# Optimization experiments

Measured on AMD Instinct MI355X. Metric: run time of the kernel, lower is better.

The kernel has to match this reference:

```python
import jax, jax.numpy as jnp
import numpy as np

B, L, HID, H, DH = 1, 2048, 1024, 16, 64
KW = 2  # d_conv
EPS = float(np.finfo(np.float32).eps)  # torch RMSNorm eps=None -> dtype eps


def _causal_dw_conv(x, w, b):
    # x: (B, L, D), w: (D, K), b: (D,). Depthwise causal conv, no activation.
    Bs, Ls, D = x.shape
    K = w.shape[1]
    xp = jnp.pad(x, ((0, 0), (K - 1, 0), (0, 0)))
    out = b
    for k in range(K):
        out = out + xp[:, k:k + Ls, :] * w[:, k]
    return out


def setup_inputs() -> dict:
    key = jax.random.key(0)
    ks = jax.random.split(key, 14)
    hidden_states = jax.random.normal(ks[0], (B, L, HID), jnp.float32)
    # masked_fill(attention_mask != 0, -inf): True above diagonal (future masked)
    attention_mask = jnp.triu(jnp.ones((L, L), dtype=bool), 1)[None, None]
    all_dim = 3 * H * DH  # q_size + 2*kv_size with KVH == H
    qkv_w = jax.random.normal(ks[1], (all_dim, HID), jnp.float32) * 0.02
    q_conv_w = jax.random.normal(ks[2], (H * DH, KW), jnp.float32) * 0.5
    q_conv_b = jax.random.normal(ks[3], (H * DH,), jnp.float32) * 0.02
    k_conv_w = jax.random.normal(ks[4], (H * DH, KW), jnp.float32) * 0.5
    k_conv_b = jax.random.normal(ks[5], (H * DH,), jnp.float32) * 0.02
    v_conv_w = jax.random.normal(ks[6], (H * DH, KW), jnp.float32) * 0.5
    v_conv_b = jax.random.normal(ks[7], (H * DH,), jnp.float32) * 0.02
    norm_w = jnp.ones((DH,), jnp.float32)
    A_log = jnp.log(jax.random.uniform(ks[8], (H,), jnp.float32, 1.0, 16.0))
    dt0 = jnp.exp(jax.random.uniform(ks[9], (H,), jnp.float32)
                  * (np.log(0.1) - np.log(0.001)) + np.log(0.001))
    dt0 = jnp.clip(dt0, 1e-4)
    dt_bias = dt0 + jnp.log(-jnp.expm1(-dt0))  # inverse softplus init
    dt_proj_w = jax.random.normal(ks[10], (H, HID), jnp.float32) * 0.02
    dt_proj_b = jnp.zeros((H,), jnp.float32)
    o_w = jax.random.normal(ks[11], (HID, H * DH), jnp.float32) * 0.02
    order_coeff = jnp.ones((1, H, 1, 1), jnp.float32)  # 1/cumprod(arange(1,2))
    return dict(hidden_states=hidden_states, attention_mask=attention_mask,
                qkv_w=qkv_w, q_conv_w=q_conv_w, q_conv_b=q_conv_b,
                k_conv_w=k_conv_w, k_conv_b=k_conv_b, v_conv_w=v_conv_w,
                v_conv_b=v_conv_b, norm_w=norm_w, A_log=A_log, dt_bias=dt_bias,
                dt_proj_w=dt_proj_w, dt_proj_b=dt_proj_b, o_w=o_w,
                order_coeff=order_coeff)


def reference(hidden_states, attention_mask, qkv_w, q_conv_w, q_conv_b,
              k_conv_w, k_conv_b, v_conv_w, v_conv_b, norm_w, A_log, dt_bias,
              dt_proj_w, dt_proj_b, o_w, order_coeff):
    qs = H * DH
    qkv = hidden_states @ qkv_w.T                    # (B, L, 3*H*DH)
    q = _causal_dw_conv(qkv[..., :qs], q_conv_w, q_conv_b)
    k = _causal_dw_conv(qkv[..., qs:2 * qs], k_conv_w, k_conv_b)
    v = _causal_dw_conv(qkv[..., 2 * qs:], v_conv_w, v_conv_b)
    # split heads -> (B, H, L, DH)
    q = q.reshape(B, L, H, DH).transpose(0, 2, 1, 3)
    k = k.reshape(B, L, H, DH).transpose(0, 2, 1, 3)
    v = v.reshape(B, L, H, DH).transpose(0, 2, 1, 3)
    # SSM-style gate: dt (B, L, H)
    dt = jax.nn.softplus(hidden_states @ dt_proj_w.T + dt_proj_b + dt_bias)
    v = v * jnp.swapaxes(dt, 1, 2)[..., None]        # value scaled by dt
    A = -jnp.exp(A_log)[None, None, :] * dt          # (B, L, H)
    A_cumsum = jnp.swapaxes(jnp.cumsum(A, axis=1), 1, 2)  # (B, H, L)
    diff = A_cumsum[:, :, :, None] - A_cumsum[:, :, None, :]  # (B, H, L, L)
    A_mask = jnp.exp(jnp.where(attention_mask, -jnp.inf, diff))
    # order == 1: Taylor series reduces to a single gated linear term
    scores = jnp.einsum('bhld,bhmd->bhlm', q, k) * A_mask * (1.0 / order_coeff)
    out = scores @ v                                  # (B, H, L, DH)
    # RMSNorm over head_dim
    out = out * jax.lax.rsqrt(jnp.mean(out * out, -1, keepdims=True) + EPS) * norm_w
    out = out.transpose(0, 2, 1, 3).reshape(B, L, H * DH)
    return out @ o_w.T
```

## Files before the change

kernel.cpp:

```cpp
#include <hip/hip_runtime.h>
#include <hip/hip_bf16.h>

#define L_SEQ 2048
#define HIDN  1024
#define NH    16
#define DHD   64
#define QKV_N 3072

typedef float f4 __attribute__((ext_vector_type(4)));
typedef __bf16 bf16x8 __attribute__((ext_vector_type(8)));
typedef _Float16 half8 __attribute__((ext_vector_type(8)));
typedef unsigned int u32x2 __attribute__((ext_vector_type(2)));

union H8 {
  half8 h;
  u32x2 u2[2];
  uint4 u4;
};

__device__ __forceinline__ float b2f(unsigned short u) {
  union { unsigned int i; float f; } c; c.i = ((unsigned int)u) << 16; return c.f;
}
__device__ __forceinline__ unsigned short f2b(float f) {
  union { float f; unsigned int i; } c; c.f = f;
  unsigned int r = c.i + 0x7FFFu + ((c.i >> 16) & 1u);
  return (unsigned short)(r >> 16);
}
__device__ __forceinline__ unsigned short f2h(float f) {
  union { _Float16 h; unsigned short u; } c; c.h = (_Float16)f; return c.u;
}
__device__ __forceinline__ void unpack8(uint4 u, float* f) {
  unsigned int w[4] = {u.x, u.y, u.z, u.w};
#pragma unroll
  for (int i = 0; i < 4; ++i) {
    union { unsigned int i_; float f_; } lo, hi;
    lo.i_ = w[i] << 16;
    hi.i_ = w[i] & 0xffff0000u;
    f[2 * i] = lo.f_; f[2 * i + 1] = hi.f_;
  }
}

__global__ __launch_bounds__(256) void prep_kernel(
    const void* hs, const void* qkvw, const void* ow, const void* dtw,
    const void* qw, const void* qb, const void* kw, const void* kb,
    const void* vw, const void* vb, const void* nw, const void* al,
    const void* dtb, const void* dpb, const void* oc,
    unsigned short* __restrict__ hs_b, unsigned short* __restrict__ qkvw_b,
    unsigned short* __restrict__ ow_b, unsigned short* __restrict__ dtw_b,
    float* __restrict__ smallf, int* __restrict__ flag)
{
  __shared__ int cnt;
  if (threadIdx.x == 0) cnt = 0;
  __syncthreads();
  {
    const unsigned short* p = (const unsigned short*)hs;
    int c = 0;
    for (int i = threadIdx.x; i < 8192; i += 256)
      if (((p[i] >> 7) & 0xFFu) >= 140u) c++;
    atomicAdd(&cnt, c);
  }
  __syncthreads();
  const int f = (cnt >= 32) ? 1 : 0;
  if (blockIdx.x == 0 && threadIdx.x == 0) *flag = f;

  const int tid = blockIdx.x * 256 + threadIdx.x;
  const int nth = gridDim.x * 256;
  for (int i = tid; i < 1576960; i += nth) {
    const void* src; unsigned short* dst; int off;
    if (i < 524288)       { src = hs;   dst = hs_b;   off = i; }
    else if (i < 1310720) { src = qkvw; dst = qkvw_b; off = i - 524288; }
    else if (i < 1572864) { src = ow;   dst = ow_b;   off = i - 1310720; }
    else                  { src = dtw;  dst = dtw_b;  off = i - 1572864; }
    const int e = off * 4;
    if (f) {
      f4 v = *(const f4*)((const float*)src + e);
      ushort4 o;
      o.x = f2b(v[0]); o.y = f2b(v[1]); o.z = f2b(v[2]); o.w = f2b(v[3]);
      *(ushort4*)(dst + e) = o;
    } else {
      *(uint2*)(dst + e) = *(const uint2*)((const unsigned short*)src + e);
    }
  }
  const void* ptrs[11] = {qw, qb, kw, kb, vw, vb, nw, al, dtb, dpb, oc};
  const int sizes[11] = {2048, 1024, 2048, 1024, 2048, 1024, 64, 16, 16, 16, 16};
  int off = 0;
  for (int a = 0; a < 11; ++a) {
    for (int i = tid; i < sizes[a]; i += nth)
      smallf[off + i] = f ? ((const float*)ptrs[a])[i]
                          : b2f(((const unsigned short*)ptrs[a])[i]);
    off += sizes[a];
  }
}

__global__ __launch_bounds__(256) void gemm128(
    const unsigned short* __restrict__ A, const unsigned short* __restrict__ B,
    float* __restrict__ C, int M, int N, int K)
{
  __shared__ __align__(16) unsigned short As[128 * 40];
  __shared__ __align__(16) unsigned short Bs[128 * 40];
  const int t = threadIdx.x;
  const int w = t >> 6, lane = t & 63;
  const int quad = lane >> 4, l16 = lane & 15;
  const int wr = w >> 1, wc = w & 1;
  const int m0 = blockIdx.y * 128, n0 = blockIdx.x * 128;
  const int srow = t >> 1;
  const int scol = (t & 1) * 16;

  f4 acc[4][4];
#pragma unroll
  for (int i = 0; i < 4; ++i)
#pragma unroll
    for (int j = 0; j < 4; ++j) acc[i][j] = (f4){0.f, 0.f, 0.f, 0.f};

  const unsigned short* apg = A + (size_t)(m0 + srow) * K + scol;
  const unsigned short* bpg = B + (size_t)(n0 + srow) * K + scol;
  uint4 a0 = *(const uint4*)apg,       a1 = *(const uint4*)(apg + 8);
  uint4 b0 = *(const uint4*)bpg,       b1 = *(const uint4*)(bpg + 8);

  for (int k0 = 0; k0 < K; k0 += 32) {
    __syncthreads();
    *(uint4*)&As[srow * 40 + scol]     = a0;
    *(uint4*)&As[srow * 40 + scol + 8] = a1;
    *(uint4*)&Bs[srow * 40 + scol]     = b0;
    *(uint4*)&Bs[srow * 40 + scol + 8] = b1;
    __syncthreads();
    if (k0 + 32 < K) {
      a0 = *(const uint4*)(apg + k0 + 32); a1 = *(const uint4*)(apg + k0 + 40);
      b0 = *(const uint4*)(bpg + k0 + 32); b1 = *(const uint4*)(bpg + k0 + 40);
    }
    bf16x8 aF[4], bF[4];
#pragma unroll
    for (int i = 0; i < 4; ++i)
      aF[i] = *(const bf16x8*)&As[(wr * 64 + i * 16 + l16) * 40 + quad * 8];
#pragma unroll
    for (int j = 0; j < 4; ++j)
      bF[j] = *(const bf16x8*)&Bs[(wc * 64 + j * 16 + l16) * 40 + quad * 8];
#pragma unroll
    for (int i = 0; i < 4; ++i)
#pragma unroll
      for (int j = 0; j < 4; ++j)
        acc[i][j] = __builtin_amdgcn_mfma_f32_16x16x32_bf16(aF[i], bF[j], acc[i][j], 0, 0, 0);
  }

#pragma unroll
  for (int i = 0; i < 4; ++i)
#pragma unroll
    for (int j = 0; j < 4; ++j)
#pragma unroll
      for (int r = 0; r < 4; ++r) {
        int m = m0 + wr * 64 + i * 16 + quad * 4 + r;
        int n = n0 + wc * 64 + j * 16 + l16;
        C[(size_t)m * N + n] = acc[i][j][r];
      }
}

template <int MODE>
__global__ __launch_bounds__(256) void gemm_bt(
    const unsigned short* __restrict__ A, const unsigned short* __restrict__ B,
    void* __restrict__ Cv, int M, int N, int K, const int* __restrict__ flag)
{
  __shared__ __align__(16) short As[64 * 40];
  __shared__ __align__(16) short Bs[64 * 40];
  const int t = threadIdx.x;
  const int wave = t >> 6, lane = t & 63;
  const int quad = lane >> 4, l16 = lane & 15;
  const int m0 = blockIdx.y * 64, n0 = blockIdx.x * 64;
  const int srow = t >> 2, scol = (t & 3) * 8;
  f4 acc[4];
#pragma unroll
  for (int i = 0; i < 4; ++i) acc[i] = (f4){0.f, 0.f, 0.f, 0.f};
  const unsigned short* ap = A + (size_t)(m0 + srow) * K + scol;
  const unsigned short* bp = B + (size_t)(n0 + srow) * K + scol;
  for (int k0 = 0; k0 < K; k0 += 32) {
    uint4 av = *(const uint4*)(ap + k0);
    uint4 bv = *(const uint4*)(bp + k0);
    __syncthreads();
    *(uint4*)&As[srow * 40 + scol] = av;
    *(uint4*)&Bs[srow * 40 + scol] = bv;
    __syncthreads();
    bf16x8 af = *(const bf16x8*)&As[(wave * 16 + l16) * 40 + quad * 8];
#pragma unroll
    for (int nt = 0; nt < 4; ++nt) {
      bf16x8 bf = *(const bf16x8*)&Bs[(nt * 16 + l16) * 40 + quad * 8];
      acc[nt] = __builtin_amdgcn_mfma_f32_16x16x32_bf16(af, bf, acc[nt], 0, 0, 0);
    }
  }
  const int outf32 = (MODE == 0) ? 1 : (*flag ? 1 : 0);
#pragma unroll
  for (int nt = 0; nt < 4; ++nt) {
#pragma unroll
    for (int r = 0; r < 4; ++r) {
      int m = m0 + wave * 16 + quad * 4 + r;
      int n = n0 + nt * 16 + l16;
      if (outf32) ((float*)Cv)[(size_t)m * N + n] = acc[nt][r];
      else        ((unsigned short*)Cv)[(size_t)m * N + n] = f2b(acc[nt][r]);
    }
  }
}

__global__ __launch_bounds__(256) void dt_kernel(
    const unsigned short* __restrict__ hs,
    const unsigned short* __restrict__ dtw,
    const float* __restrict__ smallf,
    float* __restrict__ dt_out, float* __restrict__ A_out)
{
  const int l = blockIdx.x;
  const int t = threadIdx.x, wave = t >> 6, lane = t & 63;
  const unsigned short* hp = hs + (size_t)l * HIDN + lane * 16;
  float hv[16];
  unpack8(*(const uint4*)hp, hv);
  unpack8(*(const uint4*)(hp + 8), hv + 8);
#pragma unroll
  for (int hh = 0; hh < 4; ++hh) {
    const int hd = wave * 4 + hh;
    const unsigned short* wp = dtw + (size_t)hd * HIDN + lane * 16;
    float wv[16];
    unpack8(*(const uint4*)wp, wv);
    unpack8(*(const uint4*)(wp + 8), wv + 8);
    float p = 0.f;
#pragma unroll
    for (int i = 0; i < 16; ++i) p += hv[i] * wv[i];
#pragma unroll
    for (int off = 32; off > 0; off >>= 1) p += __shfl_down(p, off);
    if (lane == 0) {
      float z = p + smallf[9312 + hd] + smallf[9296 + hd];
      float dtv = (z > 20.f) ? z : log1pf(expf(z));
      dt_out[l * NH + hd] = dtv;
      A_out[l * NH + hd] = -expf(smallf[9280 + hd]) * dtv;
    }
  }
}

__global__ __launch_bounds__(64) void cumsum_kernel(const float* __restrict__ A_in,
                                                    float* __restrict__ Ac)
{
  const int h = blockIdx.x;
  const int lane = threadIdx.x;
  const int base = lane * 32;
  float run = 0.f;
  for (int i = 0; i < 32; ++i) run += A_in[(base + i) * NH + h];
  float incl = run;
#pragma unroll
  for (int off = 1; off < 64; off <<= 1) {
    float n = __shfl_up(incl, off);
    if (lane >= off) incl += n;
  }
  float r2 = incl - run;
  for (int i = 0; i < 32; ++i) {
    r2 += A_in[(base + i) * NH + h];
    Ac[h * L_SEQ + base + i] = r2;
  }
}

__global__ __launch_bounds__(256) void conv_kernel(
    const float* __restrict__ qkv, const float* __restrict__ smallf,
    const float* __restrict__ dt, unsigned short* __restrict__ qc)
{
  const int idx = blockIdx.x * 256 + threadIdx.x;
  const int l = idx / (QKV_N / 4);
  const int c = (idx % (QKV_N / 4)) * 4;
  f4 xc = *(const f4*)&qkv[(size_t)l * QKV_N + c];
  f4 xp = (f4){0.f, 0.f, 0.f, 0.f};
  if (l > 0) xp = *(const f4*)&qkv[(size_t)(l - 1) * QKV_N + c];
  const float* w; const float* b; int cb;
  if (c < HIDN)          { w = smallf;        b = smallf + 2048; cb = c; }
  else if (c < 2 * HIDN) { w = smallf + 3072; b = smallf + 5120; cb = c - HIDN; }
  else                   { w = smallf + 6144; b = smallf + 8192; cb = c - 2 * HIDN; }
  f4 o;
#pragma unroll
  for (int j = 0; j < 4; ++j)
    o[j] = b[cb + j] + xp[j] * w[(cb + j) * 2] + xc[j] * w[(cb + j) * 2 + 1];
  if (c >= 2 * HIDN) {
    const int hh = (c - 2 * HIDN) >> 6;
    o *= dt[l * NH + hh];
  }
  ushort4 st;
  st.x = f2h(o[0]); st.y = f2h(o[1]); st.z = f2h(o[2]); st.w = f2h(o[3]);
  *(ushort4*)&qc[(size_t)l * QKV_N + c] = st;
}

__global__ __launch_bounds__(256) void transpose_v(
    const unsigned short* __restrict__ qc, unsigned short* __restrict__ vt)
{
  const int h = blockIdx.y;
  const int l0 = blockIdx.x * 64;
  const int t = threadIdx.x;
  const int srow = t >> 2, cc = t & 3;
  __shared__ __align__(16) unsigned short Ts[64 * 68];
  const unsigned short* gp =
      qc + (size_t)(l0 + srow) * QKV_N + 2 * HIDN + h * DHD + cc * 16;
  uint4 a = *(const uint4*)gp;
  uint4 b = *(const uint4*)(gp + 8);
  *(uint4*)&Ts[srow * 68 + cc * 16] = a;
  *(uint4*)&Ts[srow * 68 + cc * 16 + 8] = b;
  __syncthreads();
  __align__(16) unsigned short o[16];
#pragma unroll
  for (int j = 0; j < 16; ++j) o[j] = Ts[(cc * 16 + j) * 68 + srow];
  unsigned short* op = vt + ((size_t)h * DHD + srow) * L_SEQ + l0 + cc * 16;
  *(uint4*)op = *(const uint4*)&o[0];
  *(uint4*)(op + 8) = *(const uint4*)&o[8];
}

__global__ __launch_bounds__(256) void attn_kernel(
    const unsigned short* __restrict__ qc,
    const unsigned short* __restrict__ vt,
    const float* __restrict__ Ac,
    const float* __restrict__ smallf,
    unsigned short* __restrict__ attn_out)
{
  const int h  = blockIdx.y;
  const int bx = blockIdx.x;
  const int jj = bx >> 1;
  const int base = (bx & 1) ? jj : (31 - jj);
  const int lt = (h < 8) ? base : (31 - base);
  const int t  = threadIdx.x;
  const int w    = t >> 6;
  const int lane = t & 63;
  const int l16  = lane & 15;
  const int quad = lane >> 4;
  const int srow = t >> 2;
  const int cc   = t & 3;

  __shared__ __align__(16) unsigned short K_lds[2][64 * 68];
  __shared__ __align__(16) unsigned short V_lds[2][64 * 68];
  __shared__ __align__(16) unsigned short S_lds[64 * 68];

  const int l0 = lt * 64;
  const float rc = 1.0f / smallf[9328 + h];
  const float* Acp = Ac + h * L_SEQ;

  H8 qf0, qf1;
  {
    const unsigned short* qp =
        qc + (size_t)(l0 + w * 16 + l16) * QKV_N + h * DHD + quad * 8;
    qf0.u4 = *(const uint4*)qp;
    qf1.u4 = *(const uint4*)(qp + 32);
  }
  float alv[4];
#pragma unroll
  for (int r = 0; r < 4; ++r) alv[r] = Acp[l0 + w * 16 + quad * 4 + r];

  f4 acc[4];
#pragma unroll
  for (int i = 0; i < 4; ++i) acc[i] = (f4){0.f, 0.f, 0.f, 0.f};

  const unsigned short* kgp =
      qc + (size_t)srow * QKV_N + HIDN + h * DHD + cc * 16;
  const unsigned short* vgp =
      vt + ((size_t)h * DHD + srow) * L_SEQ + cc * 16;

  const int swo = srow * 68 + cc * 16;

  uint4 k0v = *(const uint4*)kgp,       k1v = *(const uint4*)(kgp + 8);
  uint4 v0v = *(const uint4*)vgp,       v1v = *(const uint4*)(vgp + 8);
  float amv[4];
#pragma unroll
  for (int nt = 0; nt < 4; ++nt) amv[nt] = Acp[nt * 16 + l16];

  *(u32x2*)&K_lds[0][swo]      = (u32x2){k0v.x, k0v.y};
  *(u32x2*)&K_lds[0][swo + 4]  = (u32x2){k0v.z, k0v.w};
  *(u32x2*)&K_lds[0][swo + 8]  = (u32x2){k1v.x, k1v.y};
  *(u32x2*)&K_lds[0][swo + 12] = (u32x2){k1v.z, k1v.w};
  *(u32x2*)&V_lds[0][swo]      = (u32x2){v0v.x, v0v.y};
  *(u32x2*)&V_lds[0][swo + 4]  = (u32x2){v0v.z, v0v.w};
  *(u32x2*)&V_lds[0][swo + 8]  = (u32x2){v1v.x, v1v.y};
  *(u32x2*)&V_lds[0][swo + 12] = (u32x2){v1v.z, v1v.w};
  __syncthreads();

  int cur = 0;
  for (int it = 0; it <= lt; ++it) {
    uint4 nk0 = k0v, nk1 = k1v, nv0 = v0v, nv1 = v1v;
    float namv[4];
    const bool more = (it < lt);
    if (more) {
      const unsigned short* kp = kgp + (size_t)(it + 1) * 64 * QKV_N;
      const unsigned short* vp = vgp + (size_t)(it + 1) * 64;
      nk0 = *(const uint4*)kp; nk1 = *(const uint4*)(kp + 8);
      nv0 = *(const uint4*)vp; nv1 = *(const uint4*)(vp + 8);
#pragma unroll
      for (int nt = 0; nt < 4; ++nt)
        namv[nt] = Acp[(it + 1) * 64 + nt * 16 + l16];
    }

    f4 s[4];
#pragma unroll
    for (int i = 0; i < 4; ++i) s[i] = (f4){0.f, 0.f, 0.f, 0.f};
#pragma unroll
    for (int ks = 0; ks < 2; ++ks) {
      H8 qk = ks ? qf1 : qf0;
#pragma unroll
      for (int nt = 0; nt < 4; ++nt) {
        H8 kf;
        const int ko = (nt * 16 + l16) * 68 + ks * 32 + quad * 8;
        kf.u2[0] = *(const u32x2*)&K_lds[cur][ko];
        kf.u2[1] = *(const u32x2*)&K_lds[cur][ko + 4];
        s[nt] = __builtin_amdgcn_mfma_f32_16x16x32_f16(qk.h, kf.h, s[nt], 0, 0, 0);
      }
    }
    const int m0 = it * 64;
#pragma unroll
    for (int nt = 0; nt < 4; ++nt) {
      const int mg = m0 + nt * 16 + l16;
      const float am = amv[nt];
#pragma unroll
      for (int r = 0; r < 4; ++r) {
        const int lg = l0 + w * 16 + quad * 4 + r;
        float val = (mg <= lg) ? s[nt][r] * __expf(alv[r] - am) * rc : 0.0f;
        S_lds[(w * 16 + quad * 4 + r) * 68 + nt * 16 + l16] = f2h(val);
      }
    }
#pragma unroll
    for (int ks = 0; ks < 2; ++ks) {
      H8 sa;
      const int so = (w * 16 + l16) * 68 + ks * 32 + quad * 8;
      sa.u2[0] = *(const u32x2*)&S_lds[so];
      sa.u2[1] = *(const u32x2*)&S_lds[so + 4];
#pragma unroll
      for (int db = 0; db < 4; ++db) {
        H8 vb;
        const int vo = (db * 16 + l16) * 68 + ks * 32 + quad * 8;
        vb.u2[0] = *(const u32x2*)&V_lds[cur][vo];
        vb.u2[1] = *(const u32x2*)&V_lds[cur][vo + 4];
        acc[db] = __builtin_amdgcn_mfma_f32_16x16x32_f16(sa.h, vb.h, acc[db], 0, 0, 0);
      }
    }
    if (more) {
      unsigned short* Kl = K_lds[cur ^ 1];
      unsigned short* Vl = V_lds[cur ^ 1];
      *(u32x2*)&Kl[swo]      = (u32x2){nk0.x, nk0.y};
      *(u32x2*)&Kl[swo + 4]  = (u32x2){nk0.z, nk0.w};
      *(u32x2*)&Kl[swo + 8]  = (u32x2){nk1.x, nk1.y};
      *(u32x2*)&Kl[swo + 12] = (u32x2){nk1.z, nk1.w};
      *(u32x2*)&Vl[swo]      = (u32x2){nv0.x, nv0.y};
      *(u32x2*)&Vl[swo + 4]  = (u32x2){nv0.z, nv0.w};
      *(u32x2*)&Vl[swo + 8]  = (u32x2){nv1.x, nv1.y};
      *(u32x2*)&Vl[swo + 12] = (u32x2){nv1.z, nv1.w};
#pragma unroll
      for (int nt = 0; nt < 4; ++nt) amv[nt] = namv[nt];
      __syncthreads();
      cur ^= 1;
    }
  }

#pragma unroll
  for (int r = 0; r < 4; ++r) {
    float p = acc[0][r] * acc[0][r] + acc[1][r] * acc[1][r]
            + acc[2][r] * acc[2][r] + acc[3][r] * acc[3][r];
#pragma unroll
    for (int off = 1; off < 16; off <<= 1) p += __shfl_xor(p, off);
    const float rn = rsqrtf(p * (1.0f / 64.0f) + 1.1920928955078125e-07f);
    unsigned short* op =
        attn_out + (size_t)(l0 + w * 16 + quad * 4 + r) * HIDN + h * DHD + l16;
#pragma unroll
    for (int ds = 0; ds < 4; ++ds)
      op[ds * 16] = f2b(acc[ds][r] * rn * smallf[9216 + ds * 16 + l16]);
  }
}

extern "C" void kernel_launch(void* const* d_in, const int* in_sizes, int n_in,
                              void* d_out, int out_size, void* d_ws, size_t ws_size,
                              hipStream_t stream)
{
  (void)in_sizes; (void)n_in; (void)out_size; (void)ws_size;
  const void* hs        = d_in[0];
  const void* qkv_w     = d_in[2];
  const void* q_conv_w  = d_in[3];
  const void* q_conv_b  = d_in[4];
  const void* k_conv_w  = d_in[5];
  const void* k_conv_b  = d_in[6];
  const void* v_conv_w  = d_in[7];
  const void* v_conv_b  = d_in[8];
  const void* norm_w    = d_in[9];
  const void* A_log     = d_in[10];
  const void* dt_bias   = d_in[11];
  const void* dt_proj_w = d_in[12];
  const void* dt_proj_b = d_in[13];
  const void* o_w       = d_in[14];
  const void* ordc      = d_in[15];

  char* ws = (char*)d_ws;
  int* flag             = (int*)ws;
  unsigned short* hs_b  = (unsigned short*)(ws + 256);
  unsigned short* qkvw_b= (unsigned short*)(ws + 4194560);
  unsigned short* ow_b  = (unsigned short*)(ws + 10486016);
  unsigned short* dtw_b = (unsigned short*)(ws + 12583168);
  float* smallf         = (float*)(ws + 12615936);
  float* qkv            = (float*)(ws + 12653568);
  unsigned short* qc_h  = (unsigned short*)(ws + 37819392);
  float* dtbuf          = (float*)(ws + 62985216);
  float* Abuf           = (float*)(ws + 63116288);
  float* Acum           = (float*)(ws + 63247360);
  unsigned short* attnb = (unsigned short*)(ws + 63378432);
  unsigned short* vt_h  = (unsigned short*)(ws + 67572736);

  prep_kernel<<<1024, 256, 0, stream>>>(
      hs, qkv_w, o_w, dt_proj_w,
      q_conv_w, q_conv_b, k_conv_w, k_conv_b, v_conv_w, v_conv_b,
      norm_w, A_log, dt_bias, dt_proj_b, ordc,
      hs_b, qkvw_b, ow_b, dtw_b, smallf, flag);

  gemm128<<<dim3(QKV_N / 128, L_SEQ / 128), 256, 0, stream>>>(
      hs_b, qkvw_b, qkv, L_SEQ, QKV_N, HIDN);
  dt_kernel<<<L_SEQ, 256, 0, stream>>>(hs_b, dtw_b, smallf, dtbuf, Abuf);
  cumsum_kernel<<<NH, 64, 0, stream>>>(Abuf, Acum);
  conv_kernel<<<(L_SEQ * QKV_N / 4) / 256, 256, 0, stream>>>(qkv, smallf, dtbuf, qc_h);
  transpose_v<<<dim3(L_SEQ / 64, NH), 256, 0, stream>>>(qc_h, vt_h);
  attn_kernel<<<dim3(32, NH), 256, 0, stream>>>(qc_h, vt_h, Acum, smallf, attnb);
  gemm_bt<1><<<dim3(HIDN / 64, L_SEQ / 64), 256, 0, stream>>>(
      attnb, ow_b, d_out, L_SEQ, HIDN, HIDN, flag);
}
```

Baseline: 244.0 us.

## Fuse dt projection into QKV GEMM and merge conv with V transpose

Appends the 16 dt_proj rows, zero-padded to 3200 columns, to the QKV weight so the dt projection is computed inside the main GEMM. The separate dt kernel goes away, and softplus plus A are computed in the cumsum kernel. The conv kernel now also scales, convolves and transposes V directly into the transposed buffer, removing the transpose_v launch and the V round-trip. The attention grid mapping is changed to interleave heads for load balance. The cost is a wider GEMM with 128 extra padded columns and a single-block-per-head cumsum that now does the softplus work.

```diff
diff --git a/kernel.cpp b/kernel.cpp
--- a/kernel.cpp
+++ b/kernel.cpp
@@ -5,7 +5,8 @@
 #define HIDN  1024
 #define NH    16
 #define DHD   64
-#define QKV_N 3072
+#define QKV_P 3200
+#define QC_S  2048
 
 typedef float f4 __attribute__((ext_vector_type(4)));
 typedef __bf16 bf16x8 __attribute__((ext_vector_type(8)));
@@ -28,16 +29,6 @@
 }
 __device__ __forceinline__ unsigned short f2h(float f) {
   union { _Float16 h; unsigned short u; } c; c.h = (_Float16)f; return c.u;
-}
-__device__ __forceinline__ void unpack8(uint4 u, float* f) {
-  unsigned int w[4] = {u.x, u.y, u.z, u.w};
-#pragma unroll
-  for (int i = 0; i < 4; ++i) {
-    union { unsigned int i_; float f_; } lo, hi;
-    lo.i_ = w[i] << 16;
-    hi.i_ = w[i] & 0xffff0000u;
-    f[2 * i] = lo.f_; f[2 * i + 1] = hi.f_;
-  }
 }
 
 __global__ __launch_bounds__(256) void prep_kernel(
@@ -46,7 +37,7 @@
     const void* vw, const void* vb, const void* nw, const void* al,
     const void* dtb, const void* dpb, const void* oc,
     unsigned short* __restrict__ hs_b, unsigned short* __restrict__ qkvw_b,
-    unsigned short* __restrict__ ow_b, unsigned short* __restrict__ dtw_b,
+    unsigned short* __restrict__ ow_b,
     float* __restrict__ smallf, int* __restrict__ flag)
 {
   __shared__ int cnt;
@@ -65,12 +56,16 @@
 
   const int tid = blockIdx.x * 256 + threadIdx.x;
   const int nth = gridDim.x * 256;
-  for (int i = tid; i < 1576960; i += nth) {
+  for (int i = tid; i < 1605632; i += nth) {
     const void* src; unsigned short* dst; int off;
     if (i < 524288)       { src = hs;   dst = hs_b;   off = i; }
     else if (i < 1310720) { src = qkvw; dst = qkvw_b; off = i - 524288; }
-    else if (i < 1572864) { src = ow;   dst = ow_b;   off = i - 1310720; }
-    else                  { src = dtw;  dst = dtw_b;  off = i - 1572864; }
+    else if (i < 1314816) { src = dtw;  dst = qkvw_b + 3072 * 1024; off = i - 1310720; }
+    else if (i < 1343488) {
+      *(ushort4*)(qkvw_b + 3088 * 1024 + (i - 1314816) * 4) = (ushort4){0, 0, 0, 0};
+      continue;
+    }
+    else                  { src = ow;   dst = ow_b;   off = i - 1343488; }
     const int e = off * 4;
     if (f) {
       f4 v = *(const f4*)((const float*)src + e);
@@ -198,47 +193,26 @@
   }
 }
 
-__global__ __launch_bounds__(256) void dt_kernel(
-    const unsigned short* __restrict__ hs,
-    const unsigned short* __restrict__ dtw,
-    const float* __restrict__ smallf,
-    float* __restrict__ dt_out, float* __restrict__ A_out)
-{
-  const int l = blockIdx.x;
-  const int t = threadIdx.x, wave = t >> 6, lane = t & 63;
-  const unsigned short* hp = hs + (size_t)l * HIDN + lane * 16;
-  float hv[16];
-  unpack8(*(const uint4*)hp, hv);
-  unpack8(*(const uint4*)(hp + 8), hv + 8);
-#pragma unroll
-  for (int hh = 0; hh < 4; ++hh) {
-    const int hd = wave * 4 + hh;
-    const unsigned short* wp = dtw + (size_t)hd * HIDN + lane * 16;
-    float wv[16];
-    unpack8(*(const uint4*)wp, wv);
-    unpack8(*(const uint4*)(wp + 8), wv + 8);
-    float p = 0.f;
-#pragma unroll
-    for (int i = 0; i < 16; ++i) p += hv[i] * wv[i];
-#pragma unroll
-    for (int off = 32; off > 0; off >>= 1) p += __shfl_down(p, off);
-    if (lane == 0) {
-      float z = p + smallf[9312 + hd] + smallf[9296 + hd];
-      float dtv = (z > 20.f) ? z : log1pf(expf(z));
-      dt_out[l * NH + hd] = dtv;
-      A_out[l * NH + hd] = -expf(smallf[9280 + hd]) * dtv;
-    }
-  }
-}
-
-__global__ __launch_bounds__(64) void cumsum_kernel(const float* __restrict__ A_in,
-                                                    float* __restrict__ Ac)
+__global__ __launch_bounds__(64) void cumsum_kernel(
+    const float* __restrict__ qkvf, const float* __restrict__ smallf,
+    float* __restrict__ dt_out, float* __restrict__ Ac)
 {
   const int h = blockIdx.x;
   const int lane = threadIdx.x;
   const int base = lane * 32;
+  const float dpb = smallf[9312 + h], dtb = smallf[9296 + h];
+  const float nal = -expf(smallf[9280 + h]);
+  float Av[32];
   float run = 0.f;
-  for (int i = 0; i < 32; ++i) run += A_in[(base + i) * NH + h];
+#pragma unroll
+  for (int i = 0; i < 32; ++i) {
+    const int l = base + i;
+    float z = qkvf[(size_t)l * QKV_P + 3072 + h] + dpb + dtb;
+    float dtv = (z > 20.f) ? z : log1pf(expf(z));
+    dt_out[l * NH + h] = dtv;
+    Av[i] = nal * dtv;
+    run += Av[i];
+  }
   float incl = run;
 #pragma unroll
   for (int off = 1; off < 64; off <<= 1) {
@@ -246,60 +220,72 @@
     if (lane >= off) incl += n;
   }
   float r2 = incl - run;
+#pragma unroll
   for (int i = 0; i < 32; ++i) {
-    r2 += A_in[(base + i) * NH + h];
+    r2 += Av[i];
     Ac[h * L_SEQ + base + i] = r2;
   }
 }
 
 __global__ __launch_bounds__(256) void conv_kernel(
-    const float* __restrict__ qkv, const float* __restrict__ smallf,
-    const float* __restrict__ dt, unsigned short* __restrict__ qc)
-{
-  const int idx = blockIdx.x * 256 + threadIdx.x;
-  const int l = idx / (QKV_N / 4);
-  const int c = (idx % (QKV_N / 4)) * 4;
-  f4 xc = *(const f4*)&qkv[(size_t)l * QKV_N + c];
-  f4 xp = (f4){0.f, 0.f, 0.f, 0.f};
-  if (l > 0) xp = *(const f4*)&qkv[(size_t)(l - 1) * QKV_N + c];
-  const float* w; const float* b; int cb;
-  if (c < HIDN)          { w = smallf;        b = smallf + 2048; cb = c; }
-  else if (c < 2 * HIDN) { w = smallf + 3072; b = smallf + 5120; cb = c - HIDN; }
-  else                   { w = smallf + 6144; b = smallf + 8192; cb = c - 2 * HIDN; }
-  f4 o;
-#pragma unroll
-  for (int j = 0; j < 4; ++j)
-    o[j] = b[cb + j] + xp[j] * w[(cb + j) * 2] + xc[j] * w[(cb + j) * 2 + 1];
-  if (c >= 2 * HIDN) {
-    const int hh = (c - 2 * HIDN) >> 6;
-    o *= dt[l * NH + hh];
-  }
-  ushort4 st;
-  st.x = f2h(o[0]); st.y = f2h(o[1]); st.z = f2h(o[2]); st.w = f2h(o[3]);
-  *(ushort4*)&qc[(size_t)l * QKV_N + c] = st;
-}
-
-__global__ __launch_bounds__(256) void transpose_v(
-    const unsigned short* __restrict__ qc, unsigned short* __restrict__ vt)
-{
-  const int h = blockIdx.y;
-  const int l0 = blockIdx.x * 64;
-  const int t = threadIdx.x;
-  const int srow = t >> 2, cc = t & 3;
-  __shared__ __align__(16) unsigned short Ts[64 * 68];
-  const unsigned short* gp =
-      qc + (size_t)(l0 + srow) * QKV_N + 2 * HIDN + h * DHD + cc * 16;
-  uint4 a = *(const uint4*)gp;
-  uint4 b = *(const uint4*)(gp + 8);
-  *(uint4*)&Ts[srow * 68 + cc * 16] = a;
-  *(uint4*)&Ts[srow * 68 + cc * 16 + 8] = b;
-  __syncthreads();
-  __align__(16) unsigned short o[16];
-#pragma unroll
-  for (int j = 0; j < 16; ++j) o[j] = Ts[(cc * 16 + j) * 68 + srow];
-  unsigned short* op = vt + ((size_t)h * DHD + srow) * L_SEQ + l0 + cc * 16;
-  *(uint4*)op = *(const uint4*)&o[0];
-  *(uint4*)(op + 8) = *(const uint4*)&o[8];
+    const float* __restrict__ qkvf, const float* __restrict__ smallf,
+    const float* __restrict__ dt, unsigned short* __restrict__ qc,
+    unsigned short* __restrict__ vt)
+{
+  if (blockIdx.x < 4096) {
+    const int idx = blockIdx.x * 256 + threadIdx.x;
+    const int l = idx >> 9;
+    const int c = (idx & 511) * 4;
+    f4 xc = *(const f4*)&qkvf[(size_t)l * QKV_P + c];
+    f4 xp = (f4){0.f, 0.f, 0.f, 0.f};
+    if (l > 0) xp = *(const f4*)&qkvf[(size_t)(l - 1) * QKV_P + c];
+    const float* w; const float* b; int cb;
+    if (c < HIDN) { w = smallf;        b = smallf + 2048; cb = c; }
+    else          { w = smallf + 3072; b = smallf + 5120; cb = c - HIDN; }
+    f4 o;
+#pragma unroll
+    for (int j = 0; j < 4; ++j)
+      o[j] = b[cb + j] + xp[j] * w[(cb + j) * 2] + xc[j] * w[(cb + j) * 2 + 1];
+    ushort4 st;
+    st.x = f2h(o[0]); st.y = f2h(o[1]); st.z = f2h(o[2]); st.w = f2h(o[3]);
+    *(ushort4*)&qc[(size_t)l * QC_S + c] = st;
+  } else {
+    __shared__ __align__(16) unsigned short Ts[64 * 68];
+    const int bv = blockIdx.x - 4096;
+    const int h = bv & 15;
+    const int lt0 = bv >> 4;
+    const int t = threadIdx.x;
+    const int srow = t >> 2, cc = t & 3;
+    const int l = lt0 * 64 + srow;
+    const int cb = h * 64 + cc * 16;
+    const float* w = smallf + 6144;
+    const float* b = smallf + 8192;
+    const float dtv = dt[l * NH + h];
+    const float* xcp = &qkvf[(size_t)l * QKV_P + 2048 + cb];
+    const float* xpp = &qkvf[(size_t)(l - 1) * QKV_P + 2048 + cb];
+    unsigned short o16[16];
+#pragma unroll
+    for (int g = 0; g < 4; ++g) {
+      f4 xc = *(const f4*)(xcp + g * 4);
+      f4 xp = (f4){0.f, 0.f, 0.f, 0.f};
+      if (l > 0) xp = *(const f4*)(xpp + g * 4);
+#pragma unroll
+      for (int j = 0; j < 4; ++j) {
+        const int ch = cb + g * 4 + j;
+        float o = b[ch] + xp[j] * w[ch * 2] + xc[j] * w[ch * 2 + 1];
+        o16[g * 4 + j] = f2h(o * dtv);
+      }
+    }
+    *(uint4*)&Ts[srow * 68 + cc * 16]     = *(const uint4*)&o16[0];
+    *(uint4*)&Ts[srow * 68 + cc * 16 + 8] = *(const uint4*)&o16[8];
+    __syncthreads();
+    __align__(16) unsigned short o[16];
+#pragma unroll
+    for (int j = 0; j < 16; ++j) o[j] = Ts[(cc * 16 + j) * 68 + srow];
+    unsigned short* op = vt + ((size_t)h * DHD + srow) * L_SEQ + lt0 * 64 + cc * 16;
+    *(uint4*)op = *(const uint4*)&o[0];
+    *(uint4*)(op + 8) = *(const uint4*)&o[8];
+  }
 }
 
 __global__ __launch_bounds__(256) void attn_kernel(
@@ -309,11 +295,11 @@
     const float* __restrict__ smallf,
     unsigned short* __restrict__ attn_out)
 {
-  const int h  = blockIdx.y;
-  const int bx = blockIdx.x;
-  const int jj = bx >> 1;
-  const int base = (bx & 1) ? jj : (31 - jj);
-  const int lt = (h < 8) ? base : (31 - base);
+  const int n  = blockIdx.x + 32 * blockIdx.y;
+  const int q_ = n >> 3;
+  const int h  = (n & 7) + 8 * (q_ & 1);
+  const int bxw = q_ >> 1;
+  const int lt = (bxw < 16) ? bxw : (47 - bxw);
   const int t  = threadIdx.x;
   const int w    = t >> 6;
   const int lane = t & 63;
@@ -333,7 +319,7 @@
   H8 qf0, qf1;
   {
     const unsigned short* qp =
-        qc + (size_t)(l0 + w * 16 + l16) * QKV_N + h * DHD + quad * 8;
+        qc + (size_t)(l0 + w * 16 + l16) * QC_S + h * DHD + quad * 8;
     qf0.u4 = *(const uint4*)qp;
     qf1.u4 = *(const uint4*)(qp + 32);
   }
@@ -346,7 +332,7 @@
   for (int i = 0; i < 4; ++i) acc[i] = (f4){0.f, 0.f, 0.f, 0.f};
 
   const unsigned short* kgp =
-      qc + (size_t)srow * QKV_N + HIDN + h * DHD + cc * 16;
+      qc + (size_t)srow * QC_S + HIDN + h * DHD + cc * 16;
   const unsigned short* vgp =
       vt + ((size_t)h * DHD + srow) * L_SEQ + cc * 16;
 
@@ -374,7 +360,7 @@
     float namv[4];
     const bool more = (it < lt);
     if (more) {
-      const unsigned short* kp = kgp + (size_t)(it + 1) * 64 * QKV_N;
+      const unsigned short* kp = kgp + (size_t)(it + 1) * 64 * QC_S;
       const unsigned short* vp = vgp + (size_t)(it + 1) * 64;
       nk0 = *(const uint4*)kp; nk1 = *(const uint4*)(kp + 8);
       nv0 = *(const uint4*)vp; nv1 = *(const uint4*)(vp + 8);
@@ -483,29 +469,25 @@
   int* flag             = (int*)ws;
   unsigned short* hs_b  = (unsigned short*)(ws + 256);
   unsigned short* qkvw_b= (unsigned short*)(ws + 4194560);
-  unsigned short* ow_b  = (unsigned short*)(ws + 10486016);
-  unsigned short* dtw_b = (unsigned short*)(ws + 12583168);
-  float* smallf         = (float*)(ws + 12615936);
-  float* qkv            = (float*)(ws + 12653568);
-  unsigned short* qc_h  = (unsigned short*)(ws + 37819392);
-  float* dtbuf          = (float*)(ws + 62985216);
-  float* Abuf           = (float*)(ws + 63116288);
-  float* Acum           = (float*)(ws + 63247360);
-  unsigned short* attnb = (unsigned short*)(ws + 63378432);
-  unsigned short* vt_h  = (unsigned short*)(ws + 67572736);
+  unsigned short* ow_b  = (unsigned short*)(ws + 10748160);
+  float* smallf         = (float*)(ws + 12845312);
+  float* qkvf           = (float*)(ws + 12882688);
+  unsigned short* qc_h  = (unsigned short*)(ws + 39097088);
+  float* dtbuf          = (float*)(ws + 47485696);
+  float* Acum           = (float*)(ws + 47616768);
+  unsigned short* attnb = (unsigned short*)(ws + 47747840);
+  unsigned short* vt_h  = (unsigned short*)(ws + 51942144);
 
   prep_kernel<<<1024, 256, 0, stream>>>(
       hs, qkv_w, o_w, dt_proj_w,
       q_conv_w, q_conv_b, k_conv_w, k_conv_b, v_conv_w, v_conv_b,
       norm_w, A_log, dt_bias, dt_proj_b, ordc,
-      hs_b, qkvw_b, ow_b, dtw_b, smallf, flag);
-
-  gemm128<<<dim3(QKV_N / 128, L_SEQ / 128), 256, 0, stream>>>(
-      hs_b, qkvw_b, qkv, L_SEQ, QKV_N, HIDN);
-  dt_kernel<<<L_SEQ, 256, 0, stream>>>(hs_b, dtw_b, smallf, dtbuf, Abuf);
-  cumsum_kernel<<<NH, 64, 0, stream>>>(Abuf, Acum);
-  conv_kernel<<<(L_SEQ * QKV_N / 4) / 256, 256, 0, stream>>>(qkv, smallf, dtbuf, qc_h);
-  transpose_v<<<dim3(L_SEQ / 64, NH), 256, 0, stream>>>(qc_h, vt_h);
+      hs_b, qkvw_b, ow_b, smallf, flag);
+
+  gemm128<<<dim3(QKV_P / 128, L_SEQ / 128), 256, 0, stream>>>(
+      hs_b, qkvw_b, qkvf, L_SEQ, QKV_P, HIDN);
+  cumsum_kernel<<<NH, 64, 0, stream>>>(qkvf, smallf, dtbuf, Acum);
+  conv_kernel<<<4096 + 512, 256, 0, stream>>>(qkvf, smallf, dtbuf, qc_h, vt_h);
   attn_kernel<<<dim3(32, NH), 256, 0, stream>>>(qc_h, vt_h, Acum, smallf, attnb);
   gemm_bt<1><<<dim3(HIDN / 64, L_SEQ / 64), 256, 0, stream>>>(
       attnb, ow_b, d_out, L_SEQ, HIDN, HIDN, flag);
```

Measured after the change: 247.3 us. Within noise of the previous version (+1.4%).
